# Kernel tuning notes

Hardware: AMD Instinct MI355X
Metric: run time of the kernel (lower is better)

The kernel has to match this reference:

```python
import jax, jax.numpy as jnp
from jax import lax
import numpy as np

DIM = 256
D_INNER = 2 * DIM
STATE = 64
NUM_LAYERS = 2
NUM_STACKS = 4  # 0=h_fwd, 1=h_bwd, 2=v_fwd, 3=v_bwd
SPATIAL_H = 32
SPATIAL_W = 64
EPS = 1e-5


def setup_inputs() -> dict:
    key = jax.random.key(0)
    ks = jax.random.split(key, 24)
    w = lambda k, shape: jax.random.normal(k, shape, jnp.float32) * 0.02
    B = 4
    N = SPATIAL_H * SPATIAL_W
    inp = {
        "stream_sem": jax.random.normal(ks[0], (B, N, DIM), jnp.float32),
        "stream_inst": jax.random.normal(ks[1], (B, N, DIM), jnp.float32),
        # per-stack, per-layer Mamba params
        "Wx": w(ks[2], (NUM_STACKS, NUM_LAYERS, DIM, D_INNER)),
        "Wz": w(ks[3], (NUM_STACKS, NUM_LAYERS, DIM, D_INNER)),
        "Wdt": w(ks[4], (NUM_STACKS, NUM_LAYERS, DIM, D_INNER)),
        "WB": w(ks[5], (NUM_STACKS, NUM_LAYERS, DIM, STATE)),
        "WC": w(ks[6], (NUM_STACKS, NUM_LAYERS, DIM, STATE)),
        "A_log": jax.random.normal(ks[7], (NUM_STACKS, NUM_LAYERS, D_INNER), jnp.float32) * 0.1,
        "Dskip": jnp.ones((NUM_STACKS, NUM_LAYERS, D_INNER), jnp.float32),
        "dt_bias": w(ks[8], (NUM_STACKS, NUM_LAYERS, D_INNER)),
        "Wout": w(ks[9], (NUM_STACKS, NUM_LAYERS, D_INNER, DIM)),
        "ln_s": jnp.ones((NUM_STACKS, NUM_LAYERS, DIM), jnp.float32),
        "ln_b": jnp.zeros((NUM_STACKS, NUM_LAYERS, DIM), jnp.float32),
        # merge gates for the two DirectionalBiCMS (0=horizontal, 1=vertical)
        "gate_W": w(ks[10], (2, 2 * DIM, DIM)),
        "gate_b": jnp.zeros((2, DIM), jnp.float32),
        # final sem/inst merges (Linear + LayerNorm); 0=sem, 1=inst
        "merge_W": w(ks[11], (2, 2 * DIM, DIM)),
        "merge_b": jnp.zeros((2, DIM), jnp.float32),
        "merge_ln_s": jnp.ones((2, DIM), jnp.float32),
        "merge_ln_b": jnp.zeros((2, DIM), jnp.float32),
    }
    return inp


def _layernorm(x, s, b):
    mu = jnp.mean(x, axis=-1, keepdims=True)
    xc = x - mu
    var = jnp.mean(xc * xc, axis=-1, keepdims=True)
    return xc * lax.rsqrt(var + EPS) * s + b


def _mamba_layer(x, Wx, Wz, Wdt, WB, WC, A_log, Dskip, dt_bias, Wout, ln_s, ln_b):
    # x: (Bs, L, DIM)
    h = _layernorm(x, ln_s, ln_b)
    xin = h @ Wx                                   # (Bs, L, D_INNER)
    z = h @ Wz
    dt = jax.nn.softplus(h @ Wdt + dt_bias)        # (Bs, L, D_INNER)
    Bm = h @ WB                                    # (Bs, L, STATE)
    Cm = h @ WC
    xs = jax.nn.silu(xin)
    A = -jnp.exp(A_log)                            # (D_INNER,)

    def step(hs, ins):
        dt_t, x_t, B_t, C_t = ins                  # (Bs,Di),(Bs,Di),(Bs,S),(Bs,S)
        hs = jnp.exp(dt_t * A)[..., None] * hs + (dt_t * x_t)[..., None] * B_t[:, None, :]
        y = jnp.einsum('bds,bs->bd', hs, C_t)
        return hs, y

    Bsz = x.shape[0]
    h0 = jnp.zeros((Bsz, Wx.shape[1], WB.shape[1]), x.dtype)
    mv = lambda a: jnp.moveaxis(a, 1, 0)
    _, yT = lax.scan(step, h0, (mv(dt), mv(xs), mv(Bm), mv(Cm)))
    y = jnp.moveaxis(yT, 0, 1) + Dskip * xs
    return x + (y * jax.nn.silu(z)) @ Wout


def _stack(x, si, P):
    for l in range(P['Wx'].shape[1]):
        x = _mamba_layer(x, P['Wx'][si, l], P['Wz'][si, l], P['Wdt'][si, l],
                         P['WB'][si, l], P['WC'][si, l], P['A_log'][si, l],
                         P['Dskip'][si, l], P['dt_bias'][si, l], P['Wout'][si, l],
                         P['ln_s'][si, l], P['ln_b'][si, l])
    return x


def _bicms(a, b, si_fwd, si_bwd, gW, gb, P):
    # interleave: (Bs, 2L, D)
    Bs, L, D = a.shape
    inter = jnp.stack([a, b], axis=2).reshape(Bs, 2 * L, D)
    fwd = _stack(inter, si_fwd, P)
    bwd = jnp.flip(_stack(jnp.flip(inter, axis=1), si_bwd, P), axis=1)
    gate = jax.nn.sigmoid(jnp.concatenate([fwd, bwd], axis=-1) @ gW + gb)
    merged = gate * fwd + (1.0 - gate) * bwd
    return merged[:, 0::2], merged[:, 1::2]


def _forward(stream_sem, stream_inst, P):
    B, N, D = stream_sem.shape
    H, W = SPATIAL_H, SPATIAL_W
    sem_2d = stream_sem.reshape(B, H, W, D)
    inst_2d = stream_inst.reshape(B, H, W, D)

    # horizontal (row) scans
    h_sem, h_inst = _bicms(sem_2d.reshape(B * H, W, D), inst_2d.reshape(B * H, W, D),
                           0, 1, P['gate_W'][0], P['gate_b'][0], P)
    h_sem = h_sem.reshape(B, H, W, D)
    h_inst = h_inst.reshape(B, H, W, D)

    # vertical (column) scans
    sem_cols = jnp.transpose(sem_2d, (0, 2, 1, 3)).reshape(B * W, H, D)
    inst_cols = jnp.transpose(inst_2d, (0, 2, 1, 3)).reshape(B * W, H, D)
    v_sem, v_inst = _bicms(sem_cols, inst_cols, 2, 3, P['gate_W'][1], P['gate_b'][1], P)
    v_sem = jnp.transpose(v_sem.reshape(B, W, H, D), (0, 2, 1, 3))
    v_inst = jnp.transpose(v_inst.reshape(B, W, H, D), (0, 2, 1, 3))

    fused_sem = _layernorm(jnp.concatenate([h_sem, v_sem], -1) @ P['merge_W'][0] + P['merge_b'][0],
                           P['merge_ln_s'][0], P['merge_ln_b'][0]).reshape(B, N, D)
    fused_inst = _layernorm(jnp.concatenate([h_inst, v_inst], -1) @ P['merge_W'][1] + P['merge_b'][1],
                            P['merge_ln_s'][1], P['merge_ln_b'][1]).reshape(B, N, D)
    return fused_sem, fused_inst


def reference(stream_sem, stream_inst, Wx, Wz, Wdt, WB, WC, A_log, Dskip, dt_bias, Wout,
              ln_s, ln_b, gate_W, gate_b, merge_W, merge_b, merge_ln_s, merge_ln_b):
    P = dict(Wx=Wx, Wz=Wz, Wdt=Wdt, WB=WB, WC=WC, A_log=A_log, Dskip=Dskip,
             dt_bias=dt_bias, Wout=Wout, ln_s=ln_s, ln_b=ln_b, gate_W=gate_W,
             gate_b=gate_b, merge_W=merge_W, merge_b=merge_b,
             merge_ln_s=merge_ln_s, merge_ln_b=merge_ln_b)
    return _forward(stream_sem, stream_inst, P)
```

## Files before the change

### kernel.cpp

```cpp
#include <hip/hip_runtime.h>
#include <cstdint>

#define STATE  64
#define DINNER 512

typedef __bf16  bf16x8 __attribute__((ext_vector_type(8)));
typedef float   f32x4  __attribute__((ext_vector_type(4)));
typedef float   f32x2  __attribute__((ext_vector_type(2)));

static __device__ __forceinline__ float sigmoidf_(float x){ return 1.f/(1.f+expf(-x)); }
static __device__ __forceinline__ float siluf_(float x){ return x/(1.f+expf(-x)); }
static __device__ __forceinline__ float softplusf_(float x){
    return fmaxf(x,0.f) + log1pf(expf(-fabsf(x)));
}
static __device__ __forceinline__ unsigned short f2bf(float f){
    unsigned int u = __float_as_uint(f);
    unsigned int r = (u + 0x7FFFu + ((u>>16)&1u)) >> 16;
    return (unsigned short)r;
}
static __device__ __forceinline__ float b2f(unsigned short s){
    return __uint_as_float(((unsigned int)s)<<16);
}
static __device__ __forceinline__ void gload16(const void* g, void* l){
    __builtin_amdgcn_global_load_lds(
        (const __attribute__((address_space(1))) void*)g,
        (__attribute__((address_space(3))) void*)l, 16, 0, 0);
}

__global__ __launch_bounds__(64) void prep_k(const float* __restrict__ sem,
                                             const float* __restrict__ inst,
                                             float* __restrict__ xbuf, int bi)
{
    int u = blockIdx.x;
    int lane = threadIdx.x;
    int t; long n;
    if (bi == 0) {
        int s = u >> 7; t = u & 127;
        int b = s >> 5, r = s & 31; int w = t >> 1;
        n = (long)b*2048 + r*64 + w;
    } else {
        int s = u >> 6; t = u & 63;
        int b = s >> 6, w = s & 63; int hh = t >> 1;
        n = (long)b*2048 + hh*64 + w;
    }
    const float* src = ((t & 1) ? inst : sem) + n*256 + lane*4;
    float4 v = *(const float4*)src;
    *(float4*)(xbuf + (long)u*256 + lane*4) = v;
    *(float4*)(xbuf + ((long)16384 + u)*256 + lane*4) = v;
}

template<bool BF16OUT>
__global__ __launch_bounds__(64) void ln_k(const float* __restrict__ x,
                                           void* __restrict__ outp,
                                           const float* __restrict__ sp,
                                           const float* __restrict__ bp,
                                           int pStride, int tokensPerZ)
{
    long tok = blockIdx.x;
    int z = (int)(tok / tokensPerZ);
    const float* s = sp + (long)z*pStride;
    const float* b = bp + (long)z*pStride;
    int lane = threadIdx.x;
    float4 v = *(const float4*)(x + tok*256 + lane*4);
    float sum = v.x+v.y+v.z+v.w;
    #pragma unroll
    for (int o=32;o>=1;o>>=1) sum += __shfl_xor(sum,o);
    float mu = sum * (1.f/256.f);
    float cx=v.x-mu, cy=v.y-mu, cz=v.z-mu, cw=v.w-mu;
    float vs = cx*cx+cy*cy+cz*cz+cw*cw;
    #pragma unroll
    for (int o=32;o>=1;o>>=1) vs += __shfl_xor(vs,o);
    float r = rsqrtf(vs*(1.f/256.f) + 1e-5f);
    float4 sv = *(const float4*)(s + lane*4);
    float4 bv = *(const float4*)(b + lane*4);
    float o0 = cx*r*sv.x + bv.x;
    float o1 = cy*r*sv.y + bv.y;
    float o2 = cz*r*sv.z + bv.z;
    float o3 = cw*r*sv.w + bv.w;
    if (BF16OUT) {
        ushort4 o4; o4.x=f2bf(o0); o4.y=f2bf(o1); o4.z=f2bf(o2); o4.w=f2bf(o3);
        *(ushort4*)((unsigned short*)outp + tok*256 + lane*4) = o4;
    } else {
        float4 o4; o4.x=o0; o4.y=o1; o4.z=o2; o4.w=o3;
        *(float4*)((float*)outp + tok*256 + lane*4) = o4;
    }
}

__global__ __launch_bounds__(256) void tcvt_k(const float* __restrict__ src,
                                              unsigned short* __restrict__ dst,
                                              int K, int N, long sStride, long dStride,
                                              int dRowOff, int dLd)
{
    __shared__ float t[32][33];
    int z = blockIdx.z;
    int n0 = blockIdx.x<<5, k0 = blockIdx.y<<5;
    int tx = threadIdx.x & 31, ty = threadIdx.x >> 5;
    const float* s = src + (long)z*sStride;
    #pragma unroll
    for (int i=0;i<4;i++) t[ty+8*i][tx] = s[(long)(k0+ty+8*i)*N + n0+tx];
    __syncthreads();
    unsigned short* d = dst + (long)z*dStride;
    #pragma unroll
    for (int i=0;i<4;i++)
        d[(long)(dRowOff + n0 + ty + 8*i)*dLd + k0 + tx] = f2bf(t[tx][ty+8*i]);
}

enum { EPI_SILU=0, EPI_SOFTPLUS=1, EPI_PLAINF=2, EPI_RES=3, EPI_GATE=4, EPI_BIAS=5 };

template<int MODE>
__global__ __launch_bounds__(256) void mgemm_k(
    const unsigned short* __restrict__ A, long aZ, int lda,
    const unsigned short* __restrict__ W, long wZ,
    float* __restrict__ Cf, unsigned short* __restrict__ Cb,
    int M, int K, int N,
    const float* __restrict__ p1, long s1,
    const float* __restrict__ p2,
    const float* __restrict__ p3)
{
    __shared__ __align__(16) unsigned short As[2][2048];
    __shared__ __align__(16) unsigned short Bs[2][4096];
    int z = blockIdx.z;
    const unsigned short* Az = A + (long)z*aZ;
    const unsigned short* Wz = W + (long)z*wZ;
    int bm = blockIdx.x<<6, bn = blockIdx.y<<7;
    int tid = threadIdx.x, w = tid>>6, lane = tid&63;
    int wm = w>>1, wn = w&1;
    int l15 = lane&15, l4 = lane>>4;

    f32x4 acc[2][4];
    #pragma unroll
    for (int i=0;i<2;i++)
        #pragma unroll
        for (int j=0;j<4;j++)
            acc[i][j] = (f32x4){0.f,0.f,0.f,0.f};

    auto stage = [&](int buf, int koff) {
        gload16(Az + (long)(bm + (w<<4) + l15)*lda + koff + (l4<<3), &As[buf][w<<9]);
        #pragma unroll
        for (int r = 0; r < 2; ++r) {
            int g = (r<<2) + w;
            gload16(Wz + (long)(bn + (g<<4) + l15)*K + koff + (l4<<3), &Bs[buf][g<<9]);
        }
    };

    stage(0, 0);
    __syncthreads();
    int nk = K >> 5;
    for (int t = 0; t < nk; ++t) {
        int cur = t & 1;
        if (t + 1 < nk) stage(cur ^ 1, (t + 1) << 5);
        bf16x8 a[2], b[4];
        #pragma unroll
        for (int i=0;i<2;i++)
            a[i] = *(const bf16x8*)&As[cur][(((wm<<1)+i)<<9) + (lane<<3)];
        #pragma unroll
        for (int j=0;j<4;j++)
            b[j] = *(const bf16x8*)&Bs[cur][(((wn<<2)+j)<<9) + (lane<<3)];
        #pragma unroll
        for (int i=0;i<2;i++)
            #pragma unroll
            for (int j=0;j<4;j++)
                acc[i][j] = __builtin_amdgcn_mfma_f32_16x16x32_bf16(a[i], b[j], acc[i][j], 0, 0, 0);
        __syncthreads();
    }

    #pragma unroll
    for (int i=0;i<2;i++){
        int row0 = bm + (wm<<5) + (i<<4) + (l4<<2);
        #pragma unroll
        for (int j=0;j<4;j++){
            int col = bn + (wn<<6) + (j<<4) + l15;
            #pragma unroll
            for (int tt=0;tt<4;tt++){
                int row = row0 + tt;
                long rowz = (long)z*M + row;
                float v = acc[i][j][tt];
                if (MODE == EPI_SILU) {
                    Cb[rowz*(long)N + col] = f2bf(siluf_(v));
                } else if (MODE == EPI_SOFTPLUS) {
                    Cb[rowz*(long)N + col] = f2bf(softplusf_(v + p1[(long)z*s1 + col]));
                } else if (MODE == EPI_PLAINF) {
                    Cf[rowz*(long)N + col] = v;
                } else if (MODE == EPI_RES) {
                    long rc = rowz*256 + col;
                    float o = Cf[rc] + v;
                    Cf[rc] = o;
                    Cb[(long)row*512 + (z<<8) + col] = f2bf(o);
                } else if (MODE == EPI_GATE) {
                    float gg = sigmoidf_(v + p3[col]);
                    long rl = (long)row*256 + col;
                    Cb[rl] = f2bf(gg*p1[rl] + (1.f-gg)*p2[rl]);
                } else {
                    Cf[(long)row*256 + col] = v + p1[col];
                }
            }
        }
    }
}

__global__ __launch_bounds__(256) void scan_k(
    const unsigned short* __restrict__ dtq, const unsigned short* __restrict__ xs,
    unsigned short* zg,
    const float* __restrict__ BC,
    const float* __restrict__ Alog, long aStride,
    const float* __restrict__ Dsk,
    int Bs, int Lint)
{
    __shared__ __align__(16) float bcs[4][3][128];
    int q = blockIdx.x;
    int stack = (q >= Bs) ? 1 : 0;
    int seq = q - stack*Bs;
    int tid = threadIdx.x;
    int w = tid >> 6, lane = tid & 63;
    int dl = lane & 31;
    int sh = lane >> 5;
    int d = (blockIdx.y << 7) + (w << 5) + dl;
    float Ad  = -expf(Alog[(long)stack*aStride + d]) * 1.44269504088896340736f;
    float dsk = Dsk[(long)stack*aStride + d];
    long base = (long)stack*16384 + (long)seq*Lint;
    long tok  = stack ? (base + Lint - 1) : base;
    long step = stack ? -1 : 1;

    f32x2 hs2[16];
    #pragma unroll
    for (int s=0;s<16;s++) hs2[s] = (f32x2){0.f,0.f};

    long t1 = (Lint > 1) ? tok + step : tok;
    if (lane < 32) {
        gload16(BC + tok*128 + (lane<<2), &bcs[w][0][lane<<2]);
        gload16(BC + t1*128  + (lane<<2), &bcs[w][1][lane<<2]);
    }
    float dvA = b2f(dtq[tok*DINNER + d]);
    float xvA = b2f(xs [tok*DINNER + d]);
    float zvA = b2f(zg [tok*DINNER + d]);
    float dvB = b2f(dtq[t1*DINNER + d]);
    float xvB = b2f(xs [t1*DINNER + d]);
    float zvB = b2f(zg [t1*DINNER + d]);

    int so = sh << 5;
    int cur = 0;
    for (int it = 0; it < Lint; ++it) {
        int sb = cur + 2; if (sb >= 3) sb -= 3;
        long tok2 = (it + 2 < Lint) ? tok + 2*step : tok;
        if (lane < 32) gload16(BC + tok2*128 + (lane<<2), &bcs[w][sb][lane<<2]);
        float dvC = b2f(dtq[tok2*DINNER + d]);
        float xvC = b2f(xs [tok2*DINNER + d]);
        float zvC = b2f(zg [tok2*DINNER + d]);
        asm volatile("s_waitcnt vmcnt(10)" ::: "memory");
        __builtin_amdgcn_sched_barrier(0);

        float wdec = exp2f(dvA * Ad);
        float u = dvA * xvA;
        f32x2 w2 = (f32x2){wdec, wdec};
        f32x2 u2 = (f32x2){u, u};
        const float4* B4 = (const float4*)&bcs[w][cur][so];
        const float4* C4 = (const float4*)&bcs[w][cur][64 + so];
        f32x2 acc0 = (f32x2){0.f,0.f}, acc1 = (f32x2){0.f,0.f};
        #pragma unroll
        for (int s4=0; s4<8; ++s4){
            float4 bv = B4[s4], cv = C4[s4];
            f32x2 b0 = (f32x2){bv.x, bv.y}, b1 = (f32x2){bv.z, bv.w};
            f32x2 c0 = (f32x2){cv.x, cv.y}, c1 = (f32x2){cv.z, cv.w};
            int s0 = s4<<1;
            hs2[s0]   = __builtin_elementwise_fma(w2, hs2[s0],   u2*b0);
            acc0      = __builtin_elementwise_fma(hs2[s0],   c0, acc0);
            hs2[s0+1] = __builtin_elementwise_fma(w2, hs2[s0+1], u2*b1);
            acc1      = __builtin_elementwise_fma(hs2[s0+1], c1, acc1);
        }
        f32x2 accs = acc0 + acc1;
        float part = accs.x + accs.y;
        float yv = part + __shfl_xor(part, 32);
        if (sh == 0)
            zg[tok*DINNER + d] = f2bf((yv + dsk*xvA) * zvA);

        dvA=dvB; xvA=xvB; zvA=zvB;
        dvB=dvC; xvB=xvC; zvB=zvC;
        tok += step;
        cur = cur + 1; if (cur == 3) cur = 0;
    }
}

__global__ __launch_bounds__(64) void gather_k(const unsigned short* __restrict__ mh,
                                               const unsigned short* __restrict__ mv,
                                               unsigned short* __restrict__ catsem,
                                               unsigned short* __restrict__ catinst)
{
    int n = blockIdx.x;
    int lane = threadIdx.x;
    int b = n >> 11;
    int rem = n & 2047;
    int r = rem >> 6, w = rem & 63;
    long hrow = ((long)(b*32 + r)*128 + 2*w)*256;
    long vrow = ((long)(b*64 + w)*64  + 2*r)*256;
    ushort4 hsv = *(const ushort4*)(mh + hrow + lane*4);
    ushort4 vsv = *(const ushort4*)(mv + vrow + lane*4);
    ushort4 hiv = *(const ushort4*)(mh + hrow + 256 + lane*4);
    ushort4 viv = *(const ushort4*)(mv + vrow + 256 + lane*4);
    *(ushort4*)(catsem  + (long)n*512 +       lane*4) = hsv;
    *(ushort4*)(catsem  + (long)n*512 + 256 + lane*4) = vsv;
    *(ushort4*)(catinst + (long)n*512 +       lane*4) = hiv;
    *(ushort4*)(catinst + (long)n*512 + 256 + lane*4) = viv;
}

extern "C" void kernel_launch(void* const* d_in, const int* in_sizes, int n_in,
                              void* d_out, int out_size, void* d_ws, size_t ws_size,
                              hipStream_t stream)
{
    (void)in_sizes; (void)n_in; (void)out_size; (void)ws_size;
    const float* sem  = (const float*)d_in[0];
    const float* inst = (const float*)d_in[1];
    const float* Wx   = (const float*)d_in[2];
    const float* Wz   = (const float*)d_in[3];
    const float* Wdt  = (const float*)d_in[4];
    const float* WB   = (const float*)d_in[5];
    const float* WC   = (const float*)d_in[6];
    const float* Alog = (const float*)d_in[7];
    const float* Dsk  = (const float*)d_in[8];
    const float* dtb  = (const float*)d_in[9];
    const float* Wo   = (const float*)d_in[10];
    const float* lns  = (const float*)d_in[11];
    const float* lnb  = (const float*)d_in[12];
    const float* gW   = (const float*)d_in[13];
    const float* gb   = (const float*)d_in[14];
    const float* mW   = (const float*)d_in[15];
    const float* mb   = (const float*)d_in[16];
    const float* mlns = (const float*)d_in[17];
    const float* mlnb = (const float*)d_in[18];
    float* out = (float*)d_out;

    char* base = (char*)d_ws;
    const long T2 = 32768;
    float* xbuf = (float*)base;                         base += T2*256*4;
    char* dtRegion = base;                              base += T2*512*4;
    unsigned short* xsb  = (unsigned short*)base;       base += T2*512*2;
    unsigned short* hb16 = (unsigned short*)base;       base += T2*256*2;
    unsigned short* gzb  = (unsigned short*)base;       base += T2*512*2;
    char* xbcRegion = base;                             base += T2*128*4;
    unsigned short* mh   = (unsigned short*)base;       base += (long)16384*256*2;
    unsigned short* mv   = (unsigned short*)base;       base += (long)16384*256*2;
    unsigned short* wxT  = (unsigned short*)base;       base += (long)8*512*256*2;
    unsigned short* wzT  = (unsigned short*)base;       base += (long)8*512*256*2;
    unsigned short* wdtT = (unsigned short*)base;       base += (long)8*512*256*2;
    unsigned short* woT  = (unsigned short*)base;       base += (long)8*256*512*2;
    unsigned short* wbc  = (unsigned short*)base;       base += (long)8*128*256*2;
    unsigned short* gwT  = (unsigned short*)base;       base += (long)2*256*512*2;
    unsigned short* mwT  = (unsigned short*)base;       base += (long)2*256*512*2;
    unsigned short* dt16 = (unsigned short*)dtRegion;
    float* logits = (float*)dtRegion;
    float* bcf = (float*)xbcRegion;
    unsigned short* xb16 = (unsigned short*)xbcRegion;
    unsigned short* cats = xsb;
    unsigned short* cati = xsb + (long)8192*512;

    dim3 t256(256);
    tcvt_k<<<dim3(16,8,8), t256, 0, stream>>>(Wx,  wxT, 256, 512, 131072L, 131072L, 0, 256);
    tcvt_k<<<dim3(16,8,8), t256, 0, stream>>>(Wz,  wzT, 256, 512, 131072L, 131072L, 0, 256);
    tcvt_k<<<dim3(16,8,8), t256, 0, stream>>>(Wdt, wdtT,256, 512, 131072L, 131072L, 0, 256);
    tcvt_k<<<dim3(8,16,8), t256, 0, stream>>>(Wo,  woT, 512, 256, 131072L, 131072L, 0, 512);
    tcvt_k<<<dim3(2,8,8),  t256, 0, stream>>>(WB,  wbc, 256, 64,  16384L,  32768L,  0, 256);
    tcvt_k<<<dim3(2,8,8),  t256, 0, stream>>>(WC,  wbc, 256, 64,  16384L,  32768L, 64, 256);
    tcvt_k<<<dim3(8,16,2), t256, 0, stream>>>(gW,  gwT, 512, 256, 131072L, 131072L, 0, 512);
    tcvt_k<<<dim3(8,16,2), t256, 0, stream>>>(mW,  mwT, 512, 256, 131072L, 131072L, 0, 512);

    for (int bi = 0; bi < 2; ++bi) {
        int Bs   = (bi == 0) ? 128 : 256;
        int Lint = (bi == 0) ? 128 : 64;
        prep_k<<<dim3(16384), dim3(64), 0, stream>>>(sem, inst, xbuf, bi);

        for (int l = 0; l < 2; ++l) {
            long slOff = (long)bi*4 + l;

            ln_k<true><<<dim3(32768), dim3(64), 0, stream>>>(
                xbuf, hb16, lns + slOff*256, lnb + slOff*256, 512, 16384);

            mgemm_k<EPI_SILU><<<dim3(256,4,2), t256, 0, stream>>>(
                hb16, 16384L*256, 256, wxT + slOff*131072, 262144L,
                nullptr, xsb, 16384, 256, 512,
                nullptr, 0L, nullptr, nullptr);

            mgemm_k<EPI_SILU><<<dim3(256,4,2), t256, 0, stream>>>(
                hb16, 16384L*256, 256, wzT + slOff*131072, 262144L,
                nullptr, gzb, 16384, 256, 512,
                nullptr, 0L, nullptr, nullptr);

            mgemm_k<EPI_SOFTPLUS><<<dim3(256,4,2), t256, 0, stream>>>(
                hb16, 16384L*256, 256, wdtT + slOff*131072, 262144L,
                nullptr, dt16, 16384, 256, 512,
                dtb + slOff*512, 1024L, nullptr, nullptr);

            mgemm_k<EPI_PLAINF><<<dim3(256,1,2), t256, 0, stream>>>(
                hb16, 16384L*256, 256, wbc + slOff*32768, 65536L,
                bcf, nullptr, 16384, 256, 128,
                nullptr, 0L, nullptr, nullptr);

            scan_k<<<dim3(2*Bs,4), t256, 0, stream>>>(
                dt16, xsb, gzb, bcf, Alog + slOff*512, 1024L,
                Dsk + slOff*512, Bs, Lint);

            mgemm_k<EPI_RES><<<dim3(256,2,2), t256, 0, stream>>>(
                gzb, 16384L*512, 512, woT + slOff*131072, 262144L,
                xbuf, xb16, 16384, 512, 256,
                nullptr, 0L, nullptr, nullptr);
        }

        mgemm_k<EPI_GATE><<<dim3(256,2,1), t256, 0, stream>>>(
            xb16, 0L, 512, gwT + (long)bi*131072, 0L,
            nullptr, (bi ? mv : mh), 16384, 512, 256,
            xbuf, 0L, xbuf + (long)16384*256, gb + bi*256);
    }

    gather_k<<<dim3(8192), dim3(64), 0, stream>>>(mh, mv, cats, cati);
    for (int mi = 0; mi < 2; ++mi) {
        const unsigned short* cat = (mi == 0) ? cats : cati;
        mgemm_k<EPI_BIAS><<<dim3(128,2,1), t256, 0, stream>>>(
            cat, 0L, 512, mwT + (long)mi*131072, 0L,
            logits, nullptr, 8192, 512, 256,
            mb + mi*256, 0L, nullptr, nullptr);
        ln_k<false><<<dim3(8192), dim3(64), 0, stream>>>(
            logits, out + (long)mi*2097152, mlns + mi*256, mlnb + mi*256, 0, 8192);
    }
}
```

Measured before the change: 1.312 ms.

## Fuse x/dt/z projection GEMMs into one launch and shrink scan blocks

Concatenates the Wx, Wdt and Wz transposed weights into one 1536-wide matrix so the three input projections run as a single GEMM launch, with the epilogue routing each column segment to its own output and activation. This removes two launches and their tail effects per layer, at the cost of a per-element segment branch in the epilogue. The scan kernel also moves from 256-thread blocks to 64-thread blocks with four times as many blocks, so each wave has its own block and its own shared buffer. That should give finer scheduling and better occupancy spread across CUs.

```diff
diff --git a/kernel.cpp b/kernel.cpp
--- a/kernel.cpp
+++ b/kernel.cpp
@@ -105,14 +105,15 @@
         d[(long)(dRowOff + n0 + ty + 8*i)*dLd + k0 + tx] = f2bf(t[tx][ty+8*i]);
 }
 
-enum { EPI_SILU=0, EPI_SOFTPLUS=1, EPI_PLAINF=2, EPI_RES=3, EPI_GATE=4, EPI_BIAS=5 };
+enum { EPI_PROJ3=0, EPI_PLAINF=1, EPI_RES=2, EPI_GATE=3, EPI_BIAS=4 };
 
 template<int MODE>
 __global__ __launch_bounds__(256) void mgemm_k(
     const unsigned short* __restrict__ A, long aZ, int lda,
     const unsigned short* __restrict__ W, long wZ,
     float* __restrict__ Cf, unsigned short* __restrict__ Cb,
-    int M, int K, int N,
+    unsigned short* __restrict__ Cb2, unsigned short* __restrict__ Cb3,
+    int M, int K,
     const float* __restrict__ p1, long s1,
     const float* __restrict__ p2,
     const float* __restrict__ p3)
@@ -175,12 +176,14 @@
                 int row = row0 + tt;
                 long rowz = (long)z*M + row;
                 float v = acc[i][j][tt];
-                if (MODE == EPI_SILU) {
-                    Cb[rowz*(long)N + col] = f2bf(siluf_(v));
-                } else if (MODE == EPI_SOFTPLUS) {
-                    Cb[rowz*(long)N + col] = f2bf(softplusf_(v + p1[(long)z*s1 + col]));
+                if (MODE == EPI_PROJ3) {
+                    int seg = col >> 9;
+                    int cin = col & 511;
+                    if (seg == 0)      Cb [rowz*512 + cin] = f2bf(siluf_(v));
+                    else if (seg == 1) Cb2[rowz*512 + cin] = f2bf(softplusf_(v + p1[(long)z*s1 + cin]));
+                    else               Cb3[rowz*512 + cin] = f2bf(siluf_(v));
                 } else if (MODE == EPI_PLAINF) {
-                    Cf[rowz*(long)N + col] = v;
+                    Cf[rowz*128 + col] = v;
                 } else if (MODE == EPI_RES) {
                     long rc = rowz*256 + col;
                     float o = Cf[rc] + v;
@@ -198,7 +201,7 @@
     }
 }
 
-__global__ __launch_bounds__(256) void scan_k(
+__global__ __launch_bounds__(64) void scan_k(
     const unsigned short* __restrict__ dtq, const unsigned short* __restrict__ xs,
     unsigned short* zg,
     const float* __restrict__ BC,
@@ -206,15 +209,14 @@
     const float* __restrict__ Dsk,
     int Bs, int Lint)
 {
-    __shared__ __align__(16) float bcs[4][3][128];
+    __shared__ __align__(16) float bcs[3][128];
     int q = blockIdx.x;
     int stack = (q >= Bs) ? 1 : 0;
     int seq = q - stack*Bs;
-    int tid = threadIdx.x;
-    int w = tid >> 6, lane = tid & 63;
+    int lane = threadIdx.x;
     int dl = lane & 31;
     int sh = lane >> 5;
-    int d = (blockIdx.y << 7) + (w << 5) + dl;
+    int d = (blockIdx.y << 5) + dl;
     float Ad  = -expf(Alog[(long)stack*aStride + d]) * 1.44269504088896340736f;
     float dsk = Dsk[(long)stack*aStride + d];
     long base = (long)stack*16384 + (long)seq*Lint;
@@ -227,8 +229,8 @@
 
     long t1 = (Lint > 1) ? tok + step : tok;
     if (lane < 32) {
-        gload16(BC + tok*128 + (lane<<2), &bcs[w][0][lane<<2]);
-        gload16(BC + t1*128  + (lane<<2), &bcs[w][1][lane<<2]);
+        gload16(BC + tok*128 + (lane<<2), &bcs[0][lane<<2]);
+        gload16(BC + t1*128  + (lane<<2), &bcs[1][lane<<2]);
     }
     float dvA = b2f(dtq[tok*DINNER + d]);
     float xvA = b2f(xs [tok*DINNER + d]);
@@ -242,7 +244,7 @@
     for (int it = 0; it < Lint; ++it) {
         int sb = cur + 2; if (sb >= 3) sb -= 3;
         long tok2 = (it + 2 < Lint) ? tok + 2*step : tok;
-        if (lane < 32) gload16(BC + tok2*128 + (lane<<2), &bcs[w][sb][lane<<2]);
+        if (lane < 32) gload16(BC + tok2*128 + (lane<<2), &bcs[sb][lane<<2]);
         float dvC = b2f(dtq[tok2*DINNER + d]);
         float xvC = b2f(xs [tok2*DINNER + d]);
         float zvC = b2f(zg [tok2*DINNER + d]);
@@ -253,8 +255,8 @@
         float u = dvA * xvA;
         f32x2 w2 = (f32x2){wdec, wdec};
         f32x2 u2 = (f32x2){u, u};
-        const float4* B4 = (const float4*)&bcs[w][cur][so];
-        const float4* C4 = (const float4*)&bcs[w][cur][64 + so];
+        const float4* B4 = (const float4*)&bcs[cur][so];
+        const float4* C4 = (const float4*)&bcs[cur][64 + so];
         f32x2 acc0 = (f32x2){0.f,0.f}, acc1 = (f32x2){0.f,0.f};
         #pragma unroll
         for (int s4=0; s4<8; ++s4){
@@ -338,9 +340,7 @@
     char* xbcRegion = base;                             base += T2*128*4;
     unsigned short* mh   = (unsigned short*)base;       base += (long)16384*256*2;
     unsigned short* mv   = (unsigned short*)base;       base += (long)16384*256*2;
-    unsigned short* wxT  = (unsigned short*)base;       base += (long)8*512*256*2;
-    unsigned short* wzT  = (unsigned short*)base;       base += (long)8*512*256*2;
-    unsigned short* wdtT = (unsigned short*)base;       base += (long)8*512*256*2;
+    unsigned short* wP   = (unsigned short*)base;       base += (long)8*1536*256*2;
     unsigned short* woT  = (unsigned short*)base;       base += (long)8*256*512*2;
     unsigned short* wbc  = (unsigned short*)base;       base += (long)8*128*256*2;
     unsigned short* gwT  = (unsigned short*)base;       base += (long)2*256*512*2;
@@ -353,9 +353,10 @@
     unsigned short* cati = xsb + (long)8192*512;
 
     dim3 t256(256);
-    tcvt_k<<<dim3(16,8,8), t256, 0, stream>>>(Wx,  wxT, 256, 512, 131072L, 131072L, 0, 256);
-    tcvt_k<<<dim3(16,8,8), t256, 0, stream>>>(Wz,  wzT, 256, 512, 131072L, 131072L, 0, 256);
-    tcvt_k<<<dim3(16,8,8), t256, 0, stream>>>(Wdt, wdtT,256, 512, 131072L, 131072L, 0, 256);
+    const long PJ = 1536L*256;
+    tcvt_k<<<dim3(16,8,8), t256, 0, stream>>>(Wx,  wP, 256, 512, 131072L, PJ, 0,    256);
+    tcvt_k<<<dim3(16,8,8), t256, 0, stream>>>(Wdt, wP, 256, 512, 131072L, PJ, 512,  256);
+    tcvt_k<<<dim3(16,8,8), t256, 0, stream>>>(Wz,  wP, 256, 512, 131072L, PJ, 1024, 256);
     tcvt_k<<<dim3(8,16,8), t256, 0, stream>>>(Wo,  woT, 512, 256, 131072L, 131072L, 0, 512);
     tcvt_k<<<dim3(2,8,8),  t256, 0, stream>>>(WB,  wbc, 256, 64,  16384L,  32768L,  0, 256);
     tcvt_k<<<dim3(2,8,8),  t256, 0, stream>>>(WC,  wbc, 256, 64,  16384L,  32768L, 64, 256);
@@ -373,39 +374,29 @@
             ln_k<true><<<dim3(32768), dim3(64), 0, stream>>>(
                 xbuf, hb16, lns + slOff*256, lnb + slOff*256, 512, 16384);
 
-            mgemm_k<EPI_SILU><<<dim3(256,4,2), t256, 0, stream>>>(
-                hb16, 16384L*256, 256, wxT + slOff*131072, 262144L,
-                nullptr, xsb, 16384, 256, 512,
-                nullptr, 0L, nullptr, nullptr);
-
-            mgemm_k<EPI_SILU><<<dim3(256,4,2), t256, 0, stream>>>(
-                hb16, 16384L*256, 256, wzT + slOff*131072, 262144L,
-                nullptr, gzb, 16384, 256, 512,
-                nullptr, 0L, nullptr, nullptr);
-
-            mgemm_k<EPI_SOFTPLUS><<<dim3(256,4,2), t256, 0, stream>>>(
-                hb16, 16384L*256, 256, wdtT + slOff*131072, 262144L,
-                nullptr, dt16, 16384, 256, 512,
+            mgemm_k<EPI_PROJ3><<<dim3(256,12,2), t256, 0, stream>>>(
+                hb16, 16384L*256, 256, wP + slOff*PJ, 2*PJ,
+                nullptr, xsb, dt16, gzb, 16384, 256,
                 dtb + slOff*512, 1024L, nullptr, nullptr);
 
             mgemm_k<EPI_PLAINF><<<dim3(256,1,2), t256, 0, stream>>>(
                 hb16, 16384L*256, 256, wbc + slOff*32768, 65536L,
-                bcf, nullptr, 16384, 256, 128,
+                bcf, nullptr, nullptr, nullptr, 16384, 256,
                 nullptr, 0L, nullptr, nullptr);
 
-            scan_k<<<dim3(2*Bs,4), t256, 0, stream>>>(
+            scan_k<<<dim3(2*Bs,16), dim3(64), 0, stream>>>(
                 dt16, xsb, gzb, bcf, Alog + slOff*512, 1024L,
                 Dsk + slOff*512, Bs, Lint);
 
             mgemm_k<EPI_RES><<<dim3(256,2,2), t256, 0, stream>>>(
                 gzb, 16384L*512, 512, woT + slOff*131072, 262144L,
-                xbuf, xb16, 16384, 512, 256,
+                xbuf, xb16, nullptr, nullptr, 16384, 512,
                 nullptr, 0L, nullptr, nullptr);
         }
 
         mgemm_k<EPI_GATE><<<dim3(256,2,1), t256, 0, stream>>>(
             xb16, 0L, 512, gwT + (long)bi*131072, 0L,
-            nullptr, (bi ? mv : mh), 16384, 512, 256,
+            nullptr, (bi ? mv : mh), nullptr, nullptr, 16384, 512,
             xbuf, 0L, xbuf + (long)16384*256, gb + bi*256);
     }
 
@@ -414,7 +405,7 @@
         const unsigned short* cat = (mi == 0) ? cats : cati;
         mgemm_k<EPI_BIAS><<<dim3(128,2,1), t256, 0, stream>>>(
             cat, 0L, 512, mwT + (long)mi*131072, 0L,
-            logits, nullptr, 8192, 512, 256,
+            logits, nullptr, nullptr, nullptr, 8192, 512,
             mb + mi*256, 0L, nullptr, nullptr);
         ln_k<false><<<dim3(8192), dim3(64), 0, stream>>>(
             logits, out + (long)mi*2097152, mlns + mi*256, mlnb + mi*256, 0, 8192);
```

Measured after the change: 1.336 ms. About the same (+1.8%).

## Batch horizontal and vertical stacks into single merged launches per layer

Applied to the files above, without the earlier changes.

When the workspace is large enough, all four directional stacks (h_fwd, h_bwd, v_fwd, v_bwd) are processed together. Each layer's GEMMs use a z-dimension of 4 and a single scan launch covers both sequence geometries, which halves the number of kernel launches and raises per-launch parallelism. The scan kernel now derives stack, sequence length and token base per block, and the residual epilogue writes its bf16 copy in a layout that fits both modes. The cost is a larger workspace requirement, with a fallback to the old path if the workspace is too small.

```diff
diff --git a/kernel.cpp b/kernel.cpp
--- a/kernel.cpp
+++ b/kernel.cpp
@@ -185,7 +185,7 @@
                     long rc = rowz*256 + col;
                     float o = Cf[rc] + v;
                     Cf[rc] = o;
-                    Cb[(long)row*512 + (z<<8) + col] = f2bf(o);
+                    Cb[(((long)(z>>1)*16384 + row))*512 + ((z&1)<<8) + col] = f2bf(o);
                 } else if (MODE == EPI_GATE) {
                     float gg = sigmoidf_(v + p3[col]);
                     long rl = (long)row*256 + col;
@@ -202,24 +202,34 @@
     const unsigned short* __restrict__ dtq, const unsigned short* __restrict__ xs,
     unsigned short* zg,
     const float* __restrict__ BC,
-    const float* __restrict__ Alog, long aStride,
-    const float* __restrict__ Dsk,
-    int Bs, int Lint)
+    const float* __restrict__ AlogL,
+    const float* __restrict__ DskL,
+    int BsA, int LintA, int BsB, int LintB)
 {
     __shared__ __align__(16) float bcs[4][3][128];
     int q = blockIdx.x;
-    int stack = (q >= Bs) ? 1 : 0;
-    int seq = q - stack*Bs;
+    int sg, seq, Lint; long tokBase;
+    if (q < 2*BsA) {
+        int stack = (q >= BsA) ? 1 : 0;
+        seq = q - stack*BsA; sg = stack; Lint = LintA;
+        tokBase = (long)stack*BsA*LintA;
+    } else {
+        int q2 = q - 2*BsA;
+        int stack = (q2 >= BsB) ? 1 : 0;
+        seq = q2 - stack*BsB; sg = 2 + stack; Lint = LintB;
+        tokBase = (long)2*BsA*LintA + (long)stack*BsB*LintB;
+    }
+    int rev = sg & 1;
     int tid = threadIdx.x;
     int w = tid >> 6, lane = tid & 63;
     int dl = lane & 31;
     int sh = lane >> 5;
     int d = (blockIdx.y << 7) + (w << 5) + dl;
-    float Ad  = -expf(Alog[(long)stack*aStride + d]) * 1.44269504088896340736f;
-    float dsk = Dsk[(long)stack*aStride + d];
-    long base = (long)stack*16384 + (long)seq*Lint;
-    long tok  = stack ? (base + Lint - 1) : base;
-    long step = stack ? -1 : 1;
+    float Ad  = -expf(AlogL[(long)sg*1024 + d]) * 1.44269504088896340736f;
+    float dsk = DskL[(long)sg*1024 + d];
+    long base = tokBase + (long)seq*Lint;
+    long tok  = rev ? (base + Lint - 1) : base;
+    long step = rev ? -1 : 1;
 
     f32x2 hs2[16];
     #pragma unroll
@@ -306,7 +316,7 @@
                               void* d_out, int out_size, void* d_ws, size_t ws_size,
                               hipStream_t stream)
 {
-    (void)in_sizes; (void)n_in; (void)out_size; (void)ws_size;
+    (void)in_sizes; (void)n_in; (void)out_size;
     const float* sem  = (const float*)d_in[0];
     const float* inst = (const float*)d_in[1];
     const float* Wx   = (const float*)d_in[2];
@@ -327,6 +337,101 @@
     const float* mlns = (const float*)d_in[17];
     const float* mlnb = (const float*)d_in[18];
     float* out = (float*)d_out;
+
+    dim3 t256(256);
+    const bool MERGED = (ws_size >= (size_t)362283008);
+
+    if (MERGED) {
+        char* base = (char*)d_ws;
+        const long T4 = 65536;
+        float* xbuf = (float*)base;                         base += T4*256*4;
+        char* dtRegion = base;                              base += T4*512*2;
+        unsigned short* xsb  = (unsigned short*)base;       base += T4*512*2;
+        unsigned short* hb16 = (unsigned short*)base;       base += T4*256*2;
+        unsigned short* gzb  = (unsigned short*)base;       base += T4*512*2;
+        char* xbcRegion = base;                             base += T4*128*4;
+        unsigned short* mh   = (unsigned short*)base;       base += (long)16384*256*2;
+        unsigned short* mv   = (unsigned short*)base;       base += (long)16384*256*2;
+        unsigned short* wxT  = (unsigned short*)base;       base += (long)8*512*256*2;
+        unsigned short* wzT  = (unsigned short*)base;       base += (long)8*512*256*2;
+        unsigned short* wdtT = (unsigned short*)base;       base += (long)8*512*256*2;
+        unsigned short* woT  = (unsigned short*)base;       base += (long)8*256*512*2;
+        unsigned short* wbc  = (unsigned short*)base;       base += (long)8*128*256*2;
+        unsigned short* gwT  = (unsigned short*)base;       base += (long)2*256*512*2;
+        unsigned short* mwT  = (unsigned short*)base;       base += (long)2*256*512*2;
+        unsigned short* dt16 = (unsigned short*)dtRegion;
+        float* logits = (float*)dtRegion;
+        float* bcf = (float*)xbcRegion;
+        unsigned short* xb16 = (unsigned short*)xbcRegion;
+        unsigned short* cats = xsb;
+        unsigned short* cati = xsb + (long)8192*512;
+
+        tcvt_k<<<dim3(16,8,8), t256, 0, stream>>>(Wx,  wxT, 256, 512, 131072L, 131072L, 0, 256);
+        tcvt_k<<<dim3(16,8,8), t256, 0, stream>>>(Wz,  wzT, 256, 512, 131072L, 131072L, 0, 256);
+        tcvt_k<<<dim3(16,8,8), t256, 0, stream>>>(Wdt, wdtT,256, 512, 131072L, 131072L, 0, 256);
+        tcvt_k<<<dim3(8,16,8), t256, 0, stream>>>(Wo,  woT, 512, 256, 131072L, 131072L, 0, 512);
+        tcvt_k<<<dim3(2,8,8),  t256, 0, stream>>>(WB,  wbc, 256, 64,  16384L,  32768L,  0, 256);
+        tcvt_k<<<dim3(2,8,8),  t256, 0, stream>>>(WC,  wbc, 256, 64,  16384L,  32768L, 64, 256);
+        tcvt_k<<<dim3(8,16,2), t256, 0, stream>>>(gW,  gwT, 512, 256, 131072L, 131072L, 0, 512);
+        tcvt_k<<<dim3(8,16,2), t256, 0, stream>>>(mW,  mwT, 512, 256, 131072L, 131072L, 0, 512);
+
+        prep_k<<<dim3(16384), dim3(64), 0, stream>>>(sem, inst, xbuf, 0);
+        prep_k<<<dim3(16384), dim3(64), 0, stream>>>(sem, inst, xbuf + (long)32768*256, 1);
+
+        for (int l = 0; l < 2; ++l) {
+            ln_k<true><<<dim3(65536), dim3(64), 0, stream>>>(
+                xbuf, hb16, lns + l*256, lnb + l*256, 512, 16384);
+
+            mgemm_k<EPI_SILU><<<dim3(256,4,4), t256, 0, stream>>>(
+                hb16, 16384L*256, 256, wxT + (long)l*131072, 262144L,
+                nullptr, xsb, 16384, 256, 512,
+                nullptr, 0L, nullptr, nullptr);
+
+            mgemm_k<EPI_SILU><<<dim3(256,4,4), t256, 0, stream>>>(
+                hb16, 16384L*256, 256, wzT + (long)l*131072, 262144L,
+                nullptr, gzb, 16384, 256, 512,
+                nullptr, 0L, nullptr, nullptr);
+
+            mgemm_k<EPI_SOFTPLUS><<<dim3(256,4,4), t256, 0, stream>>>(
+                hb16, 16384L*256, 256, wdtT + (long)l*131072, 262144L,
+                nullptr, dt16, 16384, 256, 512,
+                dtb + l*512, 1024L, nullptr, nullptr);
+
+            mgemm_k<EPI_PLAINF><<<dim3(256,1,4), t256, 0, stream>>>(
+                hb16, 16384L*256, 256, wbc + (long)l*32768, 65536L,
+                bcf, nullptr, 16384, 256, 128,
+                nullptr, 0L, nullptr, nullptr);
+
+            scan_k<<<dim3(768,4), t256, 0, stream>>>(
+                dt16, xsb, gzb, bcf, Alog + l*512, Dsk + l*512,
+                128, 128, 256, 64);
+
+            mgemm_k<EPI_RES><<<dim3(256,2,4), t256, 0, stream>>>(
+                gzb, 16384L*512, 512, woT + (long)l*131072, 262144L,
+                xbuf, xb16, 16384, 512, 256,
+                nullptr, 0L, nullptr, nullptr);
+        }
+
+        for (int bi = 0; bi < 2; ++bi) {
+            mgemm_k<EPI_GATE><<<dim3(256,2,1), t256, 0, stream>>>(
+                xb16 + (long)bi*16384*512, 0L, 512, gwT + (long)bi*131072, 0L,
+                nullptr, (bi ? mv : mh), 16384, 512, 256,
+                xbuf + (long)bi*2*16384*256, 0L,
+                xbuf + (long)(bi*2+1)*16384*256, gb + bi*256);
+        }
+
+        gather_k<<<dim3(8192), dim3(64), 0, stream>>>(mh, mv, cats, cati);
+        for (int mi = 0; mi < 2; ++mi) {
+            const unsigned short* cat = (mi == 0) ? cats : cati;
+            mgemm_k<EPI_BIAS><<<dim3(128,2,1), t256, 0, stream>>>(
+                cat, 0L, 512, mwT + (long)mi*131072, 0L,
+                logits, nullptr, 8192, 512, 256,
+                mb + mi*256, 0L, nullptr, nullptr);
+            ln_k<false><<<dim3(8192), dim3(64), 0, stream>>>(
+                logits, out + (long)mi*2097152, mlns + mi*256, mlnb + mi*256, 0, 8192);
+        }
+        return;
+    }
 
     char* base = (char*)d_ws;
     const long T2 = 32768;
@@ -352,7 +457,6 @@
     unsigned short* cats = xsb;
     unsigned short* cati = xsb + (long)8192*512;
 
-    dim3 t256(256);
     tcvt_k<<<dim3(16,8,8), t256, 0, stream>>>(Wx,  wxT, 256, 512, 131072L, 131072L, 0, 256);
     tcvt_k<<<dim3(16,8,8), t256, 0, stream>>>(Wz,  wzT, 256, 512, 131072L, 131072L, 0, 256);
     tcvt_k<<<dim3(16,8,8), t256, 0, stream>>>(Wdt, wdtT,256, 512, 131072L, 131072L, 0, 256);
@@ -394,8 +498,8 @@
                 nullptr, 0L, nullptr, nullptr);
 
             scan_k<<<dim3(2*Bs,4), t256, 0, stream>>>(
-                dt16, xsb, gzb, bcf, Alog + slOff*512, 1024L,
-                Dsk + slOff*512, Bs, Lint);
+                dt16, xsb, gzb, bcf, Alog + slOff*512, Dsk + slOff*512,
+                Bs, Lint, 0, 0);
 
             mgemm_k<EPI_RES><<<dim3(256,2,2), t256, 0, stream>>>(
                 gzb, 16384L*512, 512, woT + slOff*131072, 262144L,
```

Measured after the change: 1.311 ms. No clear change (-0.1%).
